# Kernel tuning notes

Hardware: AMD Instinct MI355X
Metric: run time of the kernel (lower is better)

## Reference

```python
import jax, jax.numpy as jnp
import numpy as np

HEAD_DIM = 64
N_HEADS = 16
D_S = N_HEADS * HEAD_DIM  # 1024
D_Z = 128


def setup_inputs() -> dict:
    key = jax.random.key(0)
    ks = jax.random.split(key, 12)
    B, S = 1, 1024
    sc = 0.02
    return {
        "s": jax.random.normal(ks[0], (B, S, D_S), jnp.float32),
        "z": jax.random.normal(ks[1], (B, S, S, D_Z), jnp.float32),
        "wq": jax.random.normal(ks[2], (N_HEADS * HEAD_DIM, D_S), jnp.float32) * sc,
        "bq": jax.random.normal(ks[3], (N_HEADS * HEAD_DIM,), jnp.float32) * sc,
        "wk": jax.random.normal(ks[4], (N_HEADS * HEAD_DIM, D_S), jnp.float32) * sc,
        "wv": jax.random.normal(ks[5], (N_HEADS * HEAD_DIM, D_S), jnp.float32) * sc,
        "wg": jax.random.normal(ks[6], (N_HEADS * HEAD_DIM, D_S), jnp.float32) * sc,
        "z_norm_w": jnp.ones((D_Z,), jnp.float32),
        "z_norm_b": jnp.zeros((D_Z,), jnp.float32),
        "wz": jax.random.normal(ks[7], (N_HEADS, D_Z), jnp.float32) * sc,
        "wo": jax.random.normal(ks[8], (D_S, N_HEADS * HEAD_DIM), jnp.float32) * sc,
    }


def _layer_norm(x, w, b, eps=1e-5):
    mu = jnp.mean(x, axis=-1, keepdims=True)
    var = jnp.var(x, axis=-1, keepdims=True)
    return (x - mu) * jax.lax.rsqrt(var + eps) * w + b


def reference(s, z, wq, bq, wk, wv, wg, z_norm_w, z_norm_b, wz, wo):
    B, S, _ = s.shape
    H, hd = N_HEADS, HEAD_DIM
    # fused QKV projection (only q has bias in the original)
    q = (s @ wq.T + bq).reshape(B, S, H, hd)
    k = (s @ wk.T).reshape(B, S, H, hd)
    v = (s @ wv.T).reshape(B, S, H, hd)
    # pair bias: LN(z) -> linear D_Z -> H, permute to [B,H,S,S]
    zn = _layer_norm(z, z_norm_w, z_norm_b)
    bias = jnp.einsum("bijz,hz->bhij", zn, wz)  # [B,H,S,S]
    # attention with pair bias (net math: qk/sqrt(d) + bias)
    scores = jnp.einsum("bihd,bjhd->bhij", q, k) * (hd ** -0.5) + bias
    attn = jax.nn.softmax(scores, axis=-1)
    o = jnp.einsum("bhij,bjhd->bihd", attn, v).reshape(B, S, H * hd)
    # sigmoid gate then output projection
    g = jax.nn.sigmoid(s @ wg.T)
    return (o * g) @ wo.T
```

## Files before the change

### kernel.cpp

```cpp
#include <hip/hip_runtime.h>

typedef __attribute__((ext_vector_type(8))) short bf16x8;
typedef __attribute__((ext_vector_type(4))) float f32x4;

#define MFMA16(a,b,c) __builtin_amdgcn_mfma_f32_16x16x32_bf16(a,b,c,0,0,0)

__device__ __forceinline__ unsigned short f2bf(float f){
  unsigned int u = __float_as_uint(f);
  unsigned int r = (u + 0x7fffu + ((u >> 16) & 1u)) >> 16;
  return (unsigned short)r;
}
__device__ __forceinline__ float bf2f(unsigned short u){
  return __uint_as_float(((unsigned int)u) << 16);
}

__global__ __launch_bounds__(256) void prep_kernel(
    const float* __restrict__ s, const float* __restrict__ wq,
    const float* __restrict__ wk, const float* __restrict__ wv,
    const float* __restrict__ wg, const float* __restrict__ wo,
    unsigned short* __restrict__ sb, unsigned short* __restrict__ Wp,
    unsigned short* __restrict__ wob)
{
  const size_t M1 = 1u << 20;
  size_t base = ((size_t)blockIdx.x * 256 + threadIdx.x) * 4;
  const float* src; unsigned short* dst; size_t off;
  if (base < M1) { src = s; dst = sb; off = base; }
  else if (base < 5*M1) {
    size_t r = base - M1; int wsel = (int)(r >> 20);
    const float* wsrc0 = (wsel == 0) ? wq : (wsel == 1) ? wk : (wsel == 2) ? wv : wg;
    src = wsrc0; dst = Wp + ((size_t)wsel << 20); off = r & (M1 - 1);
  } else { src = wo; dst = wob; off = base - 5*M1; }
  float4 v = *(const float4*)(src + off);
  ushort4 o4;
  o4.x = f2bf(v.x); o4.y = f2bf(v.y); o4.z = f2bf(v.z); o4.w = f2bf(v.w);
  *(ushort4*)(dst + off) = o4;
}

__global__ __launch_bounds__(256) void wzprep_kernel(
    const float* __restrict__ wz, const float* __restrict__ znw,
    const float* __restrict__ znb, unsigned short* __restrict__ wzp,
    float* __restrict__ c12)
{
  __shared__ float r1[256], r2[256];
  int t = threadIdx.x; int h = t >> 4; int k0 = (t & 15) * 8;
  float p1 = 0.f, p2 = 0.f;
  for (int e = 0; e < 8; e++) {
    float wv = wz[h*128 + k0 + e];
    float w = znw[k0 + e], b = znb[k0 + e];
    wzp[h*128 + k0 + e] = f2bf(wv * w);
    p1 += wv * w; p2 += wv * b;
  }
  r1[t] = p1; r2[t] = p2;
  __syncthreads();
  if ((t & 15) == 0) {
    float s1 = 0.f, s2 = 0.f;
    for (int i = 0; i < 16; i++) { s1 += r1[t + i]; s2 += r2[t + i]; }
    c12[2*h] = s1; c12[2*h + 1] = s2;
  }
}

__global__ __launch_bounds__(256) void bias_kernel(
    const float* __restrict__ z, const unsigned short* __restrict__ wzp,
    const float* __restrict__ c12, float* __restrict__ bias)
{
  int wv = threadIdx.x >> 6, lane = threadIdx.x & 63;
  int jl = lane & 15, g = lane >> 4;
  int blk = blockIdx.x;
  int i = blk >> 4;
  int j = (blk & 15) * 64 + wv * 16 + jl;

  bf16x8 af[4];
  #pragma unroll
  for (int mk = 0; mk < 4; mk++)
    af[mk] = *(const bf16x8*)(wzp + jl*128 + mk*32 + g*8);

  const float* zp = z + ((size_t)i * 1024 + j) * 128;
  float4 zv[8];
  #pragma unroll
  for (int mk = 0; mk < 4; mk++) {
    zv[2*mk]   = *(const float4*)(zp + mk*32 + g*8);
    zv[2*mk+1] = *(const float4*)(zp + mk*32 + g*8 + 4);
  }
  float sum = 0.f, sq = 0.f;
  #pragma unroll
  for (int t = 0; t < 8; t++) {
    float4 v = zv[t];
    sum += v.x + v.y + v.z + v.w;
    sq = fmaf(v.x, v.x, fmaf(v.y, v.y, fmaf(v.z, v.z, fmaf(v.w, v.w, sq))));
  }
  sum += __shfl_xor(sum, 16); sum += __shfl_xor(sum, 32);
  sq  += __shfl_xor(sq, 16);  sq  += __shfl_xor(sq, 32);
  float mu = sum * (1.f/128.f);
  float var = sq * (1.f/128.f) - mu * mu;
  float rs = rsqrtf(var + 1e-5f);

  f32x4 D = {0.f, 0.f, 0.f, 0.f};
  #pragma unroll
  for (int mk = 0; mk < 4; mk++) {
    float4 a = zv[2*mk], b = zv[2*mk+1];
    bf16x8 t;
    t[0] = (short)f2bf(a.x); t[1] = (short)f2bf(a.y);
    t[2] = (short)f2bf(a.z); t[3] = (short)f2bf(a.w);
    t[4] = (short)f2bf(b.x); t[5] = (short)f2bf(b.y);
    t[6] = (short)f2bf(b.z); t[7] = (short)f2bf(b.w);
    D = MFMA16(af[mk], t, D);
  }
  #pragma unroll
  for (int r = 0; r < 4; r++) {
    int h = g*4 + r;
    float c1 = c12[2*h], c2 = c12[2*h + 1];
    float bvv = rs * D[r] - mu * rs * c1 + c2;
    bias[(size_t)h * 1048576 + (size_t)i * 1024 + j] = bvv;
  }
}

template<int MODE>
__global__ __launch_bounds__(256) void gemm_bf16(
    const unsigned short* __restrict__ A, const unsigned short* __restrict__ Bm,
    int M, int N, int K,
    const float* __restrict__ bq,
    unsigned short* __restrict__ qb, unsigned short* __restrict__ kb,
    unsigned short* __restrict__ vT, unsigned short* __restrict__ gb,
    float* __restrict__ outF)
{
  int lane = threadIdx.x & 63;
  int w = threadIdx.x >> 6;
  int lr = lane & 15, lg = lane >> 4;
  int row0 = blockIdx.y * 128 + (w & 1) * 64;
  int col0 = blockIdx.x * 128 + (w >> 1) * 64;
  f32x4 acc[4][4] = {};
  for (int kk = 0; kk < K; kk += 32) {
    bf16x8 af[4], bfr[4];
    #pragma unroll
    for (int t = 0; t < 4; t++)
      af[t] = *(const bf16x8*)(A + (size_t)(row0 + t*16 + lr) * K + kk + lg*8);
    #pragma unroll
    for (int t = 0; t < 4; t++)
      bfr[t] = *(const bf16x8*)(Bm + (size_t)(col0 + t*16 + lr) * K + kk + lg*8);
    #pragma unroll
    for (int a = 0; a < 4; a++)
      #pragma unroll
      for (int b = 0; b < 4; b++)
        acc[a][b] = MFMA16(af[a], bfr[b], acc[a][b]);
  }
  #pragma unroll
  for (int a = 0; a < 4; a++)
    #pragma unroll
    for (int b = 0; b < 4; b++)
      #pragma unroll
      for (int r = 0; r < 4; r++) {
        int m = row0 + a*16 + lg*4 + r;
        int n = col0 + b*16 + lr;
        float v = acc[a][b][r];
        if (MODE == 0) {
          if (n < 1024)      { v = (v + bq[n]) * 0.125f; qb[(size_t)m*1024 + n] = f2bf(v); }
          else if (n < 2048) { kb[(size_t)m*1024 + (n-1024)] = f2bf(v); }
          else if (n < 3072) { vT[(size_t)(n-2048)*1024 + m] = f2bf(v); }
          else               { float sg = 1.f / (1.f + __expf(-v)); gb[(size_t)m*1024 + (n-3072)] = f2bf(sg); }
        } else {
          outF[(size_t)m * N + n] = v;
        }
      }
}

__global__ __launch_bounds__(64) void attn_kernel(
    const unsigned short* __restrict__ qb, const unsigned short* __restrict__ kb,
    const unsigned short* __restrict__ vT, const unsigned short* __restrict__ gb,
    const float* __restrict__ bias, unsigned short* __restrict__ og)
{
  __shared__ unsigned short P[16 * 72];
  int lane = threadIdx.x;
  int jl = lane & 15, g = lane >> 4;
  int q0 = blockIdx.x * 16;
  int h = blockIdx.y;

  bf16x8 aq[2];
  #pragma unroll
  for (int kh = 0; kh < 2; kh++)
    aq[kh] = *(const bf16x8*)(qb + (size_t)(q0 + jl)*1024 + h*64 + kh*32 + g*8);

  f32x4 od[4] = {};
  float m[4], ss[4];
  #pragma unroll
  for (int r = 0; r < 4; r++) { m[r] = -1e30f; ss[r] = 0.f; }
  const float* bp = bias + (size_t)h * 1048576;

  for (int jt = 0; jt < 1024; jt += 64) {
    f32x4 sc[4] = {};
    #pragma unroll
    for (int jb = 0; jb < 4; jb++)
      #pragma unroll
      for (int kh = 0; kh < 2; kh++) {
        bf16x8 bk = *(const bf16x8*)(kb + (size_t)(jt + jb*16 + jl)*1024 + h*64 + kh*32 + g*8);
        sc[jb] = MFMA16(aq[kh], bk, sc[jb]);
      }
    #pragma unroll
    for (int jb = 0; jb < 4; jb++)
      #pragma unroll
      for (int r = 0; r < 4; r++)
        sc[jb][r] += bp[(size_t)(q0 + g*4 + r)*1024 + jt + jb*16 + jl];

    float al[4];
    #pragma unroll
    for (int r = 0; r < 4; r++) {
      float mx = fmaxf(fmaxf(sc[0][r], sc[1][r]), fmaxf(sc[2][r], sc[3][r]));
      mx = fmaxf(mx, __shfl_xor(mx, 1));
      mx = fmaxf(mx, __shfl_xor(mx, 2));
      mx = fmaxf(mx, __shfl_xor(mx, 4));
      mx = fmaxf(mx, __shfl_xor(mx, 8));
      float mn = fmaxf(m[r], mx);
      float a = __expf(m[r] - mn);
      m[r] = mn; al[r] = a;
      float rsum = 0.f;
      #pragma unroll
      for (int jb = 0; jb < 4; jb++) {
        float p = __expf(sc[jb][r] - mn);
        sc[jb][r] = p; rsum += p;
      }
      ss[r] = ss[r] * a + rsum;
    }
    #pragma unroll
    for (int db = 0; db < 4; db++)
      #pragma unroll
      for (int r = 0; r < 4; r++) od[db][r] *= al[r];

    #pragma unroll
    for (int jb = 0; jb < 4; jb++)
      #pragma unroll
      for (int r = 0; r < 4; r++)
        P[(g*4 + r)*72 + jb*16 + jl] = f2bf(sc[jb][r]);

    #pragma unroll
    for (int jh = 0; jh < 2; jh++) {
      bf16x8 ap = *(const bf16x8*)(&P[jl*72 + jh*32 + g*8]);
      #pragma unroll
      for (int db = 0; db < 4; db++) {
        bf16x8 bv = *(const bf16x8*)(vT + (size_t)(h*64 + db*16 + jl)*1024 + jt + jh*32 + g*8);
        od[db] = MFMA16(ap, bv, od[db]);
      }
    }
  }

  #pragma unroll
  for (int r = 0; r < 4; r++) {
    ss[r] += __shfl_xor(ss[r], 1); ss[r] += __shfl_xor(ss[r], 2);
    ss[r] += __shfl_xor(ss[r], 4); ss[r] += __shfl_xor(ss[r], 8);
    ss[r] = 1.f / ss[r];
  }
  #pragma unroll
  for (int db = 0; db < 4; db++)
    #pragma unroll
    for (int r = 0; r < 4; r++) {
      int q = q0 + g*4 + r;
      int d = h*64 + db*16 + jl;
      float o = od[db][r] * ss[r];
      float gv = bf2f(gb[(size_t)q*1024 + d]);
      og[(size_t)q*1024 + d] = f2bf(o * gv);
    }
}

extern "C" void kernel_launch(void* const* d_in, const int* in_sizes, int n_in,
                              void* d_out, int out_size, void* d_ws, size_t ws_size,
                              hipStream_t stream) {
  const float* s   = (const float*)d_in[0];
  const float* z   = (const float*)d_in[1];
  const float* wq  = (const float*)d_in[2];
  const float* bq  = (const float*)d_in[3];
  const float* wk  = (const float*)d_in[4];
  const float* wv  = (const float*)d_in[5];
  const float* wg  = (const float*)d_in[6];
  const float* znw = (const float*)d_in[7];
  const float* znb = (const float*)d_in[8];
  const float* wz  = (const float*)d_in[9];
  const float* wo  = (const float*)d_in[10];
  float* out = (float*)d_out;

  char* ws = (char*)d_ws;
  float*          biasb = (float*)ws;
  unsigned short* qbuf  = (unsigned short*)(ws + ((size_t)64 << 20));
  unsigned short* kbuf  = (unsigned short*)(ws + ((size_t)66 << 20));
  unsigned short* vTb   = (unsigned short*)(ws + ((size_t)68 << 20));
  unsigned short* gbuf  = (unsigned short*)(ws + ((size_t)70 << 20));
  unsigned short* ogb   = (unsigned short*)(ws + ((size_t)72 << 20));
  unsigned short* sb    = (unsigned short*)(ws + ((size_t)74 << 20));
  unsigned short* Wp    = (unsigned short*)(ws + ((size_t)76 << 20));
  unsigned short* wob   = (unsigned short*)(ws + ((size_t)84 << 20));
  unsigned short* wzp   = (unsigned short*)(ws + ((size_t)86 << 20));
  float*          c12   = (float*)(ws + ((size_t)86 << 20) + 4096);

  prep_kernel<<<6144, 256, 0, stream>>>(s, wq, wk, wv, wg, wo, sb, Wp, wob);
  wzprep_kernel<<<1, 256, 0, stream>>>(wz, znw, znb, wzp, c12);
  bias_kernel<<<16384, 256, 0, stream>>>(z, wzp, c12, biasb);
  gemm_bf16<0><<<dim3(32, 8), 256, 0, stream>>>(sb, Wp, 1024, 4096, 1024, bq,
                                                qbuf, kbuf, vTb, gbuf, nullptr);
  attn_kernel<<<dim3(64, 16), 64, 0, stream>>>(qbuf, kbuf, vTb, gbuf, biasb, ogb);
  gemm_bf16<1><<<dim3(8, 8), 256, 0, stream>>>(ogb, wob, 1024, 1024, 1024, nullptr,
                                               nullptr, nullptr, nullptr, nullptr, out);
}
```

Before: 267.6 us.

## Split attention keys across four waves with combine kernel, halve GEMM row tiles

The attention kernel now runs four waves per block, each handling a quarter of the key range (split-K flash attention). Partial outputs, row maxima and sums go to workspace and a new combine kernel merges them and applies the gate. The QK MFMA operands are swapped so each lane owns one query row, which lets the bias be read as float4 and shrinks the softmax reductions; P in shared memory uses an XOR swizzle. The GEMMs use 64-row tiles to launch more blocks. This raises occupancy on a small grid at the cost of an extra launch and extra partial-result traffic through memory.

```diff
diff --git a/kernel.cpp b/kernel.cpp
--- a/kernel.cpp
+++ b/kernel.cpp
@@ -126,25 +126,25 @@
   int lane = threadIdx.x & 63;
   int w = threadIdx.x >> 6;
   int lr = lane & 15, lg = lane >> 4;
-  int row0 = blockIdx.y * 128 + (w & 1) * 64;
+  int row0 = blockIdx.y * 64 + (w & 1) * 32;
   int col0 = blockIdx.x * 128 + (w >> 1) * 64;
-  f32x4 acc[4][4] = {};
+  f32x4 acc[2][4] = {};
   for (int kk = 0; kk < K; kk += 32) {
-    bf16x8 af[4], bfr[4];
-    #pragma unroll
-    for (int t = 0; t < 4; t++)
+    bf16x8 af[2], bfr[4];
+    #pragma unroll
+    for (int t = 0; t < 2; t++)
       af[t] = *(const bf16x8*)(A + (size_t)(row0 + t*16 + lr) * K + kk + lg*8);
     #pragma unroll
     for (int t = 0; t < 4; t++)
       bfr[t] = *(const bf16x8*)(Bm + (size_t)(col0 + t*16 + lr) * K + kk + lg*8);
     #pragma unroll
-    for (int a = 0; a < 4; a++)
+    for (int a = 0; a < 2; a++)
       #pragma unroll
       for (int b = 0; b < 4; b++)
         acc[a][b] = MFMA16(af[a], bfr[b], acc[a][b]);
   }
   #pragma unroll
-  for (int a = 0; a < 4; a++)
+  for (int a = 0; a < 2; a++)
     #pragma unroll
     for (int b = 0; b < 4; b++)
       #pragma unroll
@@ -163,16 +163,18 @@
       }
 }
 
-__global__ __launch_bounds__(64) void attn_kernel(
+__global__ __launch_bounds__(256) void attn_kernel(
     const unsigned short* __restrict__ qb, const unsigned short* __restrict__ kb,
-    const unsigned short* __restrict__ vT, const unsigned short* __restrict__ gb,
-    const float* __restrict__ bias, unsigned short* __restrict__ og)
-{
-  __shared__ unsigned short P[16 * 72];
-  int lane = threadIdx.x;
+    const unsigned short* __restrict__ vT, const float* __restrict__ bias,
+    float* __restrict__ op, float* __restrict__ ml, float* __restrict__ ll)
+{
+  __shared__ unsigned short P[4][1024];
+  int lane = threadIdx.x & 63;
+  int s = threadIdx.x >> 6;
   int jl = lane & 15, g = lane >> 4;
   int q0 = blockIdx.x * 16;
   int h = blockIdx.y;
+  unsigned short* Pw = P[s];
 
   bf16x8 aq[2];
   #pragma unroll
@@ -180,59 +182,61 @@
     aq[kh] = *(const bf16x8*)(qb + (size_t)(q0 + jl)*1024 + h*64 + kh*32 + g*8);
 
   f32x4 od[4] = {};
-  float m[4], ss[4];
-  #pragma unroll
-  for (int r = 0; r < 4; r++) { m[r] = -1e30f; ss[r] = 0.f; }
+  float m = -1e30f, ss = 0.f;
   const float* bp = bias + (size_t)h * 1048576;
 
-  for (int jt = 0; jt < 1024; jt += 64) {
+  for (int jt = s*256; jt < s*256 + 256; jt += 64) {
     f32x4 sc[4] = {};
     #pragma unroll
     for (int jb = 0; jb < 4; jb++)
       #pragma unroll
       for (int kh = 0; kh < 2; kh++) {
         bf16x8 bk = *(const bf16x8*)(kb + (size_t)(jt + jb*16 + jl)*1024 + h*64 + kh*32 + g*8);
-        sc[jb] = MFMA16(aq[kh], bk, sc[jb]);
+        sc[jb] = MFMA16(bk, aq[kh], sc[jb]);
       }
     #pragma unroll
+    for (int jb = 0; jb < 4; jb++) {
+      float4 bl = *(const float4*)(bp + (size_t)(q0 + jl)*1024 + jt + jb*16 + g*4);
+      sc[jb][0] += bl.x; sc[jb][1] += bl.y; sc[jb][2] += bl.z; sc[jb][3] += bl.w;
+    }
+
+    float mx = -1e30f;
+    #pragma unroll
     for (int jb = 0; jb < 4; jb++)
       #pragma unroll
-      for (int r = 0; r < 4; r++)
-        sc[jb][r] += bp[(size_t)(q0 + g*4 + r)*1024 + jt + jb*16 + jl];
-
-    float al[4];
-    #pragma unroll
-    for (int r = 0; r < 4; r++) {
-      float mx = fmaxf(fmaxf(sc[0][r], sc[1][r]), fmaxf(sc[2][r], sc[3][r]));
-      mx = fmaxf(mx, __shfl_xor(mx, 1));
-      mx = fmaxf(mx, __shfl_xor(mx, 2));
-      mx = fmaxf(mx, __shfl_xor(mx, 4));
-      mx = fmaxf(mx, __shfl_xor(mx, 8));
-      float mn = fmaxf(m[r], mx);
-      float a = __expf(m[r] - mn);
-      m[r] = mn; al[r] = a;
-      float rsum = 0.f;
-      #pragma unroll
-      for (int jb = 0; jb < 4; jb++) {
-        float p = __expf(sc[jb][r] - mn);
-        sc[jb][r] = p; rsum += p;
-      }
-      ss[r] = ss[r] * a + rsum;
+      for (int r = 0; r < 4; r++) mx = fmaxf(mx, sc[jb][r]);
+    mx = fmaxf(mx, __shfl_xor(mx, 16));
+    mx = fmaxf(mx, __shfl_xor(mx, 32));
+    float mn = fmaxf(m, mx);
+    float a = __expf(m - mn);
+    m = mn;
+    float rsum = 0.f;
+    #pragma unroll
+    for (int jb = 0; jb < 4; jb++) {
+      short4 pk;
+      float p0 = __expf(sc[jb][0] - mn); rsum += p0; pk.x = (short)f2bf(p0);
+      float p1 = __expf(sc[jb][1] - mn); rsum += p1; pk.y = (short)f2bf(p1);
+      float p2 = __expf(sc[jb][2] - mn); rsum += p2; pk.z = (short)f2bf(p2);
+      float p3 = __expf(sc[jb][3] - mn); rsum += p3; pk.w = (short)f2bf(p3);
+      int b = jb*2 + (g >> 1);
+      int bpz = b ^ (jl & 7);
+      *(short4*)(Pw + jl*64 + bpz*8 + (g & 1)*4) = pk;
     }
+    ss = ss * a + rsum;
+
+    float albc[4];
+    #pragma unroll
+    for (int r = 0; r < 4; r++) albc[r] = __shfl(a, g*4 + r);
     #pragma unroll
     for (int db = 0; db < 4; db++)
       #pragma unroll
-      for (int r = 0; r < 4; r++) od[db][r] *= al[r];
-
-    #pragma unroll
-    for (int jb = 0; jb < 4; jb++)
-      #pragma unroll
-      for (int r = 0; r < 4; r++)
-        P[(g*4 + r)*72 + jb*16 + jl] = f2bf(sc[jb][r]);
+      for (int r = 0; r < 4; r++) od[db][r] *= albc[r];
 
     #pragma unroll
     for (int jh = 0; jh < 2; jh++) {
-      bf16x8 ap = *(const bf16x8*)(&P[jl*72 + jh*32 + g*8]);
+      int b = jh*4 + g;
+      int bpz = b ^ (jl & 7);
+      bf16x8 ap = *(const bf16x8*)(Pw + jl*64 + bpz*8);
       #pragma unroll
       for (int db = 0; db < 4; db++) {
         bf16x8 bv = *(const bf16x8*)(vT + (size_t)(h*64 + db*16 + jl)*1024 + jt + jh*32 + g*8);
@@ -241,22 +245,64 @@
     }
   }
 
-  #pragma unroll
-  for (int r = 0; r < 4; r++) {
-    ss[r] += __shfl_xor(ss[r], 1); ss[r] += __shfl_xor(ss[r], 2);
-    ss[r] += __shfl_xor(ss[r], 4); ss[r] += __shfl_xor(ss[r], 8);
-    ss[r] = 1.f / ss[r];
-  }
+  ss += __shfl_xor(ss, 16);
+  ss += __shfl_xor(ss, 32);
+
+  size_t base = ((size_t)(s*16 + h) * 1024);
   #pragma unroll
   for (int db = 0; db < 4; db++)
     #pragma unroll
     for (int r = 0; r < 4; r++) {
       int q = q0 + g*4 + r;
-      int d = h*64 + db*16 + jl;
-      float o = od[db][r] * ss[r];
-      float gv = bf2f(gb[(size_t)q*1024 + d]);
-      og[(size_t)q*1024 + d] = f2bf(o * gv);
+      op[(base + q)*64 + db*16 + jl] = od[db][r];
     }
+  if (g == 0) {
+    ml[base + q0 + jl] = m;
+    ll[base + q0 + jl] = ss;
+  }
+}
+
+__global__ __launch_bounds__(256) void combine_kernel(
+    const float* __restrict__ op, const float* __restrict__ ml,
+    const float* __restrict__ ll, const unsigned short* __restrict__ gb,
+    unsigned short* __restrict__ og)
+{
+  int t = blockIdx.x * 256 + threadIdx.x;
+  int d4 = t & 15;
+  int q = (t >> 4) & 1023;
+  int h = t >> 14;
+
+  float mv[4], lv[4];
+  float mstar = -1e30f;
+  #pragma unroll
+  for (int s = 0; s < 4; s++) {
+    mv[s] = ml[(size_t)(s*16 + h)*1024 + q];
+    lv[s] = ll[(size_t)(s*16 + h)*1024 + q];
+    mstar = fmaxf(mstar, mv[s]);
+  }
+  float lsum = 0.f;
+  float ws[4];
+  #pragma unroll
+  for (int s = 0; s < 4; s++) {
+    ws[s] = __expf(mv[s] - mstar);
+    lsum = fmaf(ws[s], lv[s], lsum);
+  }
+  float inv = 1.f / lsum;
+
+  float4 o = {0.f, 0.f, 0.f, 0.f};
+  #pragma unroll
+  for (int s = 0; s < 4; s++) {
+    float4 p = *(const float4*)(op + ((size_t)(s*16 + h)*1024 + q)*64 + d4*4);
+    o.x = fmaf(ws[s], p.x, o.x); o.y = fmaf(ws[s], p.y, o.y);
+    o.z = fmaf(ws[s], p.z, o.z); o.w = fmaf(ws[s], p.w, o.w);
+  }
+  ushort4 gv = *(const ushort4*)(gb + (size_t)q*1024 + h*64 + d4*4);
+  ushort4 r;
+  r.x = f2bf(o.x * inv * bf2f(gv.x));
+  r.y = f2bf(o.y * inv * bf2f(gv.y));
+  r.z = f2bf(o.z * inv * bf2f(gv.z));
+  r.w = f2bf(o.w * inv * bf2f(gv.w));
+  *(ushort4*)(og + (size_t)q*1024 + h*64 + d4*4) = r;
 }
 
 extern "C" void kernel_launch(void* const* d_in, const int* in_sizes, int n_in,
@@ -287,13 +333,17 @@
   unsigned short* wob   = (unsigned short*)(ws + ((size_t)84 << 20));
   unsigned short* wzp   = (unsigned short*)(ws + ((size_t)86 << 20));
   float*          c12   = (float*)(ws + ((size_t)86 << 20) + 4096);
+  float*          opart = (float*)(ws + ((size_t)96 << 20));
+  float*          mlb   = (float*)(ws + ((size_t)112 << 20));
+  float*          llb   = (float*)(ws + ((size_t)113 << 20));
 
   prep_kernel<<<6144, 256, 0, stream>>>(s, wq, wk, wv, wg, wo, sb, Wp, wob);
   wzprep_kernel<<<1, 256, 0, stream>>>(wz, znw, znb, wzp, c12);
   bias_kernel<<<16384, 256, 0, stream>>>(z, wzp, c12, biasb);
-  gemm_bf16<0><<<dim3(32, 8), 256, 0, stream>>>(sb, Wp, 1024, 4096, 1024, bq,
-                                                qbuf, kbuf, vTb, gbuf, nullptr);
-  attn_kernel<<<dim3(64, 16), 64, 0, stream>>>(qbuf, kbuf, vTb, gbuf, biasb, ogb);
-  gemm_bf16<1><<<dim3(8, 8), 256, 0, stream>>>(ogb, wob, 1024, 1024, 1024, nullptr,
-                                               nullptr, nullptr, nullptr, nullptr, out);
-}
+  gemm_bf16<0><<<dim3(32, 16), 256, 0, stream>>>(sb, Wp, 1024, 4096, 1024, bq,
+                                                 qbuf, kbuf, vTb, gbuf, nullptr);
+  attn_kernel<<<dim3(64, 16), 256, 0, stream>>>(qbuf, kbuf, vTb, biasb, opart, mlb, llb);
+  combine_kernel<<<1024, 256, 0, stream>>>(opart, mlb, llb, gbuf, ogb);
+  gemm_bf16<1><<<dim3(8, 16), 256, 0, stream>>>(ogb, wob, 1024, 1024, 1024, nullptr,
+                                                nullptr, nullptr, nullptr, nullptr, out);
+}
```

After: 259.4 us. -3.1%, faster.
